# Optimization experiments

Hardware: AMD Instinct MI355X
Metric: run time of the kernel (lower is better)

The kernel has to match this reference:

```python
import jax, jax.numpy as jnp
import numpy as np

EMB, H, KV, HD = 2048, 32, 8, 64
G = H // KV  # group size = 4
SEQ, B = 2048, 1
EPS = 1e-6


def rms_norm(x, scale):
    # fp32 RMSNorm over last dim, no bias/centering
    v = jnp.mean(x.astype(jnp.float32) ** 2, axis=-1, keepdims=True)
    return (x * jax.lax.rsqrt(v + EPS) * scale).astype(x.dtype)


def apply_rope(x, cos, sin):
    # x: [b, h, s, d]; cos/sin: [s, d]
    d2 = x.shape[-1] // 2
    x1, x2 = x[..., :d2], x[..., d2:]
    rot = jnp.concatenate((-x2, x1), axis=-1)
    return (x * cos[None, None] + rot * sin[None, None]).astype(x.dtype)


def setup_inputs() -> dict:
    key = jax.random.key(0)
    ks = jax.random.split(key, 6)
    x = jax.random.normal(ks[0], (B, SEQ, EMB), jnp.float32)
    mask = jnp.triu(jnp.ones((SEQ, SEQ), jnp.bool_), k=1)  # causal: True = masked
    inv_freq = 1.0 / (10000.0 ** (np.arange(0, HD, 2, dtype=np.float32) / HD))
    t = np.arange(SEQ, dtype=np.float32)
    ang = np.outer(t, inv_freq)  # [seq, hd/2]
    ang = np.concatenate([ang, ang], axis=-1)  # [seq, hd]
    cos = jnp.asarray(np.cos(ang), jnp.float32)
    sin = jnp.asarray(np.sin(ang), jnp.float32)
    s = 0.02
    Wq = jax.random.normal(ks[1], (EMB, H * HD), jnp.float32) * s
    Wk = jax.random.normal(ks[2], (EMB, KV * HD), jnp.float32) * s
    Wv = jax.random.normal(ks[3], (EMB, KV * HD), jnp.float32) * s
    Wo = jax.random.normal(ks[4], (H * HD, EMB), jnp.float32) * s
    q_scale = jnp.ones((HD,), jnp.float32)
    k_scale = jnp.ones((HD,), jnp.float32)
    return {"x": x, "mask": mask, "cos": cos, "sin": sin, "Wq": Wq, "Wk": Wk,
            "Wv": Wv, "Wo": Wo, "q_scale": q_scale, "k_scale": k_scale}


def reference(x, mask, cos, sin, Wq, Wk, Wv, Wo, q_scale, k_scale):
    b, s, _ = x.shape
    q = (x @ Wq).reshape(b, s, H, HD).transpose(0, 2, 1, 3)     # [b,h,s,d]
    k = (x @ Wk).reshape(b, s, KV, HD).transpose(0, 2, 1, 3)    # [b,kv,s,d]
    v = (x @ Wv).reshape(b, s, KV, HD).transpose(0, 2, 1, 3)
    q = rms_norm(q, q_scale)
    k = rms_norm(k, k_scale)
    q = apply_rope(q, cos, sin)
    k = apply_rope(k, cos, sin)
    # grouped heads: h = kv*G + g (matches repeat_interleave along head dim)
    qg = q.reshape(b, KV, G, s, HD)
    scores = jnp.einsum('bkgqd,bkld->bkgql', qg, k) / jnp.sqrt(jnp.float32(HD))
    scores = jnp.where(mask[None, None, None], -jnp.inf, scores)
    w = jax.nn.softmax(scores.astype(jnp.float32), axis=-1).astype(q.dtype)
    ctx = jnp.einsum('bkgql,bkld->bkgqd', w, v)                 # [b,kv,g,s,d]
    ctx = ctx.reshape(b, H, s, HD).transpose(0, 2, 1, 3).reshape(b, s, H * HD)
    return ctx @ Wo
```

## Files before the change

### kernel.cpp

```cpp
#include <hip/hip_runtime.h>
#include <stdint.h>

#define EMB 2048
#define NH 32
#define NKV 8
#define HD 64
#define SEQ 2048
#define QKV_N 3072

using u16 = unsigned short;
typedef __attribute__((ext_vector_type(8))) short bf16x8;
typedef __attribute__((ext_vector_type(4))) float f32x4;
typedef __attribute__((ext_vector_type(4))) unsigned short u16x4;

__device__ inline u16 f2b(float f) {
  union { float f; unsigned u; } v; v.f = f;
  unsigned r = v.u + 0x7fffu + ((v.u >> 16) & 1u);
  return (u16)(r >> 16);
}

__device__ inline void gload16(const void* g, void* l) {
  __builtin_amdgcn_global_load_lds(
      (const __attribute__((address_space(1))) void*)g,
      (__attribute__((address_space(3))) void*)l, 16, 0, 0);
}

__global__ void cvt_x(const float* __restrict__ x, u16* __restrict__ xb) {
  int i = blockIdx.x * blockDim.x + threadIdx.x;
  float4 v = ((const float4*)x)[i];
  u16x4 o = { f2b(v.x), f2b(v.y), f2b(v.z), f2b(v.w) };
  ((u16x4*)xb)[i] = o;
}

__global__ void wtrans(const float* __restrict__ src, u16* __restrict__ dst, int R, int C) {
  __shared__ float t[64][65];
  int tx = threadIdx.x & 63, ty = threadIdx.x >> 6;
  int r0 = blockIdx.y * 64, c0 = blockIdx.x * 64;
#pragma unroll
  for (int i = 0; i < 16; ++i) {
    int r = ty * 16 + i;
    t[r][tx] = src[(size_t)(r0 + r) * C + c0 + tx];
  }
  __syncthreads();
#pragma unroll
  for (int i = 0; i < 16; ++i) {
    int r = ty * 16 + i;
    dst[(size_t)(c0 + r) * R + r0 + tx] = f2b(t[tx][r]);
  }
}

__global__ void wtrans_qkv(const float* __restrict__ Wq, const float* __restrict__ Wk,
                           const float* __restrict__ Wv, u16* __restrict__ dst) {
  __shared__ float t[64][65];
  int tx = threadIdx.x & 63, ty = threadIdx.x >> 6;
  int bx = blockIdx.x;
  int r0 = blockIdx.y * 64;
  const float* src; int C, c0;
  if (bx < 32)      { src = Wq; C = 2048; c0 = bx * 64; }
  else if (bx < 40) { src = Wk; C = 512;  c0 = (bx - 32) * 64; }
  else              { src = Wv; C = 512;  c0 = (bx - 40) * 64; }
#pragma unroll
  for (int i = 0; i < 16; ++i) {
    int r = ty * 16 + i;
    t[r][tx] = src[(size_t)(r0 + r) * C + c0 + tx];
  }
  __syncthreads();
  int drow = bx * 64;
#pragma unroll
  for (int i = 0; i < 16; ++i) {
    int r = ty * 16 + i;
    dst[(size_t)(drow + r) * 2048 + r0 + tx] = f2b(t[tx][r]);
  }
}

template<int OUT_MODE>
__global__ __launch_bounds__(256, 2)
void gemm_bt(const u16* __restrict__ A, const u16* __restrict__ BT,
             float* __restrict__ Cp, int M, int N, int K, int nwgy,
             const float* __restrict__ cosT, const float* __restrict__ sinT,
             const float* __restrict__ qsc, const float* __restrict__ ksc,
             u16* __restrict__ qb, u16* __restrict__ kb, u16* __restrict__ vT) {
  __shared__ u16 As[2][128 * 64];
  __shared__ u16 Bs[2][128 * 64];
  const int tid = threadIdx.x;
  const int w = tid >> 6, lane = tid & 63;
  const int lr = lane & 15, lg = lane >> 4;
  const int nwg = gridDim.x, cpx = nwg >> 3, pos = blockIdx.x;
  const int o = (pos & 7) * cpx + (pos >> 3);
  const int by = o % nwgy, bx = o / nwgy;
  const int m0 = by * 128, n0 = bx * 128;
  const int wm = (w >> 1) * 64, wn = (w & 1) * 64;
  f32x4 acc[4][4] = {};
  const int nk = K >> 6;

  auto STAGE = [&](int buf, int kt) {
    const int k0 = kt << 6;
    const int j = tid & 7;
#pragma unroll
    for (int i = 0; i < 4; ++i) {
      int r = i * 32 + (tid >> 3);
      int sc = (j ^ (r & 7)) * 8;
      gload16(&A[(size_t)(m0 + r) * K + k0 + sc], (char*)As[buf] + i * 4096 + w * 1024);
      gload16(&BT[(size_t)(n0 + r) * K + k0 + sc], (char*)Bs[buf] + i * 4096 + w * 1024);
    }
  };

  int cur = 0;
  STAGE(0, 0);
  asm volatile("s_waitcnt vmcnt(0)" ::: "memory");
  __syncthreads();
  for (int kt = 0; kt < nk; ++kt) {
    if (kt + 1 < nk) STAGE(cur ^ 1, kt + 1);
#pragma unroll
    for (int ks = 0; ks < 2; ++ks) {
      bf16x8 a[4], b[4];
#pragma unroll
      for (int i = 0; i < 4; ++i) {
        int row = wm + i * 16 + lr;
        a[i] = *(const bf16x8*)&As[cur][row * 64 + ((ks * 4 + lg) ^ (row & 7)) * 8];
      }
#pragma unroll
      for (int j = 0; j < 4; ++j) {
        int row = wn + j * 16 + lr;
        b[j] = *(const bf16x8*)&Bs[cur][row * 64 + ((ks * 4 + lg) ^ (row & 7)) * 8];
      }
#pragma unroll
      for (int i = 0; i < 4; ++i)
#pragma unroll
        for (int j = 0; j < 4; ++j)
          acc[i][j] = __builtin_amdgcn_mfma_f32_16x16x32_bf16(a[i], b[j], acc[i][j], 0, 0, 0);
    }
    asm volatile("s_waitcnt vmcnt(0)" ::: "memory");
    __syncthreads();
    cur ^= 1;
  }

  if (OUT_MODE == 0) {
#pragma unroll
    for (int i = 0; i < 4; ++i)
#pragma unroll
      for (int j = 0; j < 4; ++j)
#pragma unroll
        for (int r = 0; r < 4; ++r) {
          int row = m0 + wm + i * 16 + lg * 4 + r;
          int col = n0 + wn + j * 16 + lr;
          Cp[(size_t)row * N + col] = acc[i][j][r];
        }
  } else {
    const int hh = (n0 + wn) >> 6;
    if (hh < 40) {
      const float* scp = (hh < 32) ? qsc : ksc;
      u16* dst = (hh < 32) ? (qb + (size_t)hh * SEQ * HD)
                           : (kb + (size_t)(hh - 32) * SEQ * HD);
      const float qmul = (hh < 32) ? 0.125f : 1.0f;
#pragma unroll
      for (int i = 0; i < 4; ++i)
#pragma unroll
        for (int r = 0; r < 4; ++r) {
          float ssq = 0.f;
#pragma unroll
          for (int j = 0; j < 4; ++j) ssq += acc[i][j][r] * acc[i][j][r];
          ssq += __shfl_xor(ssq, 1);
          ssq += __shfl_xor(ssq, 2);
          ssq += __shfl_xor(ssq, 4);
          ssq += __shfl_xor(ssq, 8);
          float rs = rsqrtf(ssq * (1.0f / 64.0f) + 1e-6f);
          int s = m0 + wm + i * 16 + lg * 4 + r;
          float xn[4];
#pragma unroll
          for (int j = 0; j < 4; ++j) xn[j] = acc[i][j][r] * rs * scp[j * 16 + lr];
#pragma unroll
          for (int j = 0; j < 2; ++j) {
            int d = j * 16 + lr;
            float o1 = (xn[j] * cosT[s * 64 + d] - xn[j + 2] * sinT[s * 64 + d]) * qmul;
            float o2 = (xn[j + 2] * cosT[s * 64 + 32 + d] + xn[j] * sinT[s * 64 + 32 + d]) * qmul;
            dst[(size_t)s * 64 + d] = f2b(o1);
            dst[(size_t)s * 64 + 32 + d] = f2b(o2);
          }
        }
    } else {
      const int kvh = hh - 40;
      const int sbase = m0 + wm + lg * 4;
#pragma unroll
      for (int i = 0; i < 4; ++i)
#pragma unroll
        for (int j = 0; j < 4; ++j) {
          int d = j * 16 + lr;
          u16x4 pk = { f2b(acc[i][j][0]), f2b(acc[i][j][1]),
                       f2b(acc[i][j][2]), f2b(acc[i][j][3]) };
          *(u16x4*)&vT[((size_t)kvh * HD + d) * SEQ + sbase + i * 16] = pk;
        }
    }
  }
}

template<bool MASKED>
__device__ __forceinline__ void attn_step(
    const u16* __restrict__ Ks, const u16* __restrict__ VTs, u16* __restrict__ Psw,
    bf16x8 q0, bf16x8 q1, f32x4* O, float* l_acc,
    int qbase, int kbase, int lr, int lg) {
  f32x4 sc[4];
#pragma unroll
  for (int kj = 0; kj < 4; ++kj) {
    int r2 = kj * 16 + lr, sw = r2 & 7;
    bf16x8 kf0 = *(const bf16x8*)&Ks[r2 * 64 + (lg ^ sw) * 8];
    bf16x8 kf1 = *(const bf16x8*)&Ks[r2 * 64 + ((4 + lg) ^ sw) * 8];
    f32x4 z = {};
    z = __builtin_amdgcn_mfma_f32_16x16x32_bf16(q0, kf0, z, 0, 0, 0);
    z = __builtin_amdgcn_mfma_f32_16x16x32_bf16(q1, kf1, z, 0, 0, 0);
    sc[kj] = z;
  }
#pragma unroll
  for (int kj = 0; kj < 4; ++kj)
#pragma unroll
    for (int r = 0; r < 4; ++r) {
      float p;
      if (MASKED) {
        int qg = qbase + lg * 4 + r;
        int kg = kbase + kj * 16 + lr;
        p = (kg > qg) ? 0.0f : __expf(sc[kj][r] - 8.0f);
      } else {
        p = __expf(sc[kj][r] - 8.0f);
      }
      l_acc[r] += p;
      int row = lg * 4 + r, col = kj * 16 + lr;
      int sj = (col >> 3) ^ (row & 7);
      Psw[row * 64 + sj * 8 + (col & 7)] = f2b(p);
    }
#pragma unroll
  for (int ks2 = 0; ks2 < 2; ++ks2) {
    bf16x8 pa = *(const bf16x8*)&Psw[lr * 64 + ((ks2 * 4 + lg) ^ (lr & 7)) * 8];
#pragma unroll
    for (int n = 0; n < 4; ++n) {
      int r3 = n * 16 + lr, sw3 = r3 & 7;
      bf16x8 vb = *(const bf16x8*)&VTs[r3 * 64 + ((ks2 * 4 + lg) ^ sw3) * 8];
      O[n] = __builtin_amdgcn_mfma_f32_16x16x32_bf16(pa, vb, O[n], 0, 0, 0);
    }
  }
}

__global__ __launch_bounds__(256, 2)
void attn(const u16* __restrict__ qb, const u16* __restrict__ kb,
          const u16* __restrict__ vT, u16* __restrict__ ctx) {
  __shared__ u16 Ks[2][64 * 64];
  __shared__ u16 VTs[2][64 * 64];
  __shared__ u16 Ps[4][16 * 64];
  const int tid = threadIdx.x, w = tid >> 6, lane = tid & 63;
  const int lr = lane & 15, lg = lane >> 4;
  const int pos = blockIdx.x;
  const int o = (pos & 7) * 64 + (pos >> 3);
  const int h = o >> 4, p = o & 15;
  const int kvh = h >> 2;
  const int qtA = p, qtB = 31 - p;
  const int qbaseA = qtA * 64 + w * 16, qbaseB = qtB * 64 + w * 16;
  u16* Psw = &Ps[w][0];

  bf16x8 qA0 = *(const bf16x8*)&qb[((size_t)h * SEQ + qbaseA + lr) * HD + lg * 8];
  bf16x8 qA1 = *(const bf16x8*)&qb[((size_t)h * SEQ + qbaseA + lr) * HD + 32 + lg * 8];
  bf16x8 qB0 = *(const bf16x8*)&qb[((size_t)h * SEQ + qbaseB + lr) * HD + lg * 8];
  bf16x8 qB1 = *(const bf16x8*)&qb[((size_t)h * SEQ + qbaseB + lr) * HD + 32 + lg * 8];

  f32x4 OA[4] = {}, OB[4] = {};
  float lA[4] = {0.f, 0.f, 0.f, 0.f}, lB[4] = {0.f, 0.f, 0.f, 0.f};

  auto STAGE = [&](int buf, int kt) {
    const int kbase = kt * 64;
#pragma unroll
    for (int i = 0; i < 2; ++i) {
      int c = i * 256 + tid;
      int r = c >> 3, j = c & 7, sj = j ^ (r & 7);
      gload16(&kb[((size_t)kvh * SEQ + kbase + r) * HD + sj * 8],
              (char*)Ks[buf] + i * 4096 + w * 1024);
      gload16(&vT[((size_t)kvh * HD + r) * SEQ + kbase + sj * 8],
              (char*)VTs[buf] + i * 4096 + w * 1024);
    }
  };

  int cur = 0;
  STAGE(0, 0);
  asm volatile("s_waitcnt vmcnt(0)" ::: "memory");
  __syncthreads();
  for (int kt = 0; kt <= qtB; ++kt) {
    if (kt < qtB) STAGE(cur ^ 1, kt + 1);
    const int kbase = kt * 64;
    if (kt <= qtA) {
      if (kt == qtA)
        attn_step<true >(Ks[cur], VTs[cur], Psw, qA0, qA1, OA, lA, qbaseA, kbase, lr, lg);
      else
        attn_step<false>(Ks[cur], VTs[cur], Psw, qA0, qA1, OA, lA, qbaseA, kbase, lr, lg);
    }
    if (kt == qtB)
      attn_step<true >(Ks[cur], VTs[cur], Psw, qB0, qB1, OB, lB, qbaseB, kbase, lr, lg);
    else
      attn_step<false>(Ks[cur], VTs[cur], Psw, qB0, qB1, OB, lB, qbaseB, kbase, lr, lg);
    asm volatile("s_waitcnt vmcnt(0)" ::: "memory");
    __syncthreads();
    cur ^= 1;
  }

#pragma unroll
  for (int r = 0; r < 4; ++r) {
#pragma unroll
    for (int off = 1; off < 16; off <<= 1) {
      lA[r] += __shfl_xor(lA[r], off);
      lB[r] += __shfl_xor(lB[r], off);
    }
  }
#pragma unroll
  for (int n = 0; n < 4; ++n)
#pragma unroll
    for (int r = 0; r < 4; ++r) {
      int sA = qbaseA + lg * 4 + r;
      ctx[(size_t)sA * 2048 + h * 64 + n * 16 + lr] = f2b(OA[n][r] / lA[r]);
      int sB = qbaseB + lg * 4 + r;
      ctx[(size_t)sB * 2048 + h * 64 + n * 16 + lr] = f2b(OB[n][r] / lB[r]);
    }
}

extern "C" void kernel_launch(void* const* d_in, const int* in_sizes, int n_in,
                              void* d_out, int out_size, void* d_ws, size_t ws_size,
                              hipStream_t stream) {
  const float* x    = (const float*)d_in[0];
  const float* cosT = (const float*)d_in[2];
  const float* sinT = (const float*)d_in[3];
  const float* Wq   = (const float*)d_in[4];
  const float* Wk   = (const float*)d_in[5];
  const float* Wv   = (const float*)d_in[6];
  const float* Wo   = (const float*)d_in[7];
  const float* qsc  = (const float*)d_in[8];
  const float* ksc  = (const float*)d_in[9];
  float* out = (float*)d_out;

  char* wsp = (char*)d_ws;
  u16*   xb    = (u16*)(wsp);
  u16*   WqkvT = (u16*)(wsp + ((size_t)8  << 20));
  u16*   WoT   = (u16*)(wsp + ((size_t)20 << 20));
  u16*   qbuf  = (u16*)(wsp + ((size_t)28 << 20));
  u16*   kbuf  = (u16*)(wsp + ((size_t)36 << 20));
  u16*   vTbuf = (u16*)(wsp + ((size_t)38 << 20));
  u16*   ctxb  = (u16*)(wsp + ((size_t)40 << 20));

  cvt_x<<<4096, 256, 0, stream>>>(x, xb);
  wtrans_qkv<<<dim3(48, 32), 256, 0, stream>>>(Wq, Wk, Wv, WqkvT);
  wtrans<<<dim3(32, 32), 256, 0, stream>>>(Wo, WoT, 2048, 2048);

  gemm_bt<2><<<384, 256, 0, stream>>>(xb, WqkvT, nullptr, 2048, 3072, 2048, 16,
                                      cosT, sinT, qsc, ksc, qbuf, kbuf, vTbuf);
  attn<<<512, 256, 0, stream>>>(qbuf, kbuf, vTbuf, ctxb);
  gemm_bt<0><<<256, 256, 0, stream>>>((const u16*)ctxb, WoT, out, 2048, 2048, 2048, 16,
                                      nullptr, nullptr, nullptr, nullptr,
                                      nullptr, nullptr, nullptr);
}
```

Before: 139.4 us.

## Deepen attention K/V prefetch to 4 buffers and share K/V fragments across tiles

The attention loop now uses four LDS buffers for K and V with a prefetch distance of two tiles, waiting on partial vmcnt instead of draining all loads each iteration. The two query tiles (A and B) are processed in one fused step, so each K/V fragment is read from LDS once and feeds both sets of MFMAs. Softmax switches to exp2 with log2(e) folded into the Q scaling, and the P conversion to bf16 uses a cheaper rounding. The goal is less load-latency stall and fewer LDS reads. The cost is more LDS per block (80KB), which may limit occupancy, and slightly different rounding of P.

```diff
diff --git a/kernel.cpp b/kernel.cpp
--- a/kernel.cpp
+++ b/kernel.cpp
@@ -13,10 +13,17 @@
 typedef __attribute__((ext_vector_type(4))) float f32x4;
 typedef __attribute__((ext_vector_type(4))) unsigned short u16x4;
 
+#define MFMA16(a, b, c) __builtin_amdgcn_mfma_f32_16x16x32_bf16(a, b, c, 0, 0, 0)
+#define EXP2_C8 11.5415603f
+
 __device__ inline u16 f2b(float f) {
   union { float f; unsigned u; } v; v.f = f;
   unsigned r = v.u + 0x7fffu + ((v.u >> 16) & 1u);
   return (u16)(r >> 16);
+}
+__device__ inline u16 f2b_fast(float f) {
+  union { float f; unsigned u; } v; v.f = f;
+  return (u16)((v.u + 0x8000u) >> 16);
 }
 
 __device__ inline void gload16(const void* g, void* l) {
@@ -128,7 +135,7 @@
       for (int i = 0; i < 4; ++i)
 #pragma unroll
         for (int j = 0; j < 4; ++j)
-          acc[i][j] = __builtin_amdgcn_mfma_f32_16x16x32_bf16(a[i], b[j], acc[i][j], 0, 0, 0);
+          acc[i][j] = MFMA16(a[i], b[j], acc[i][j]);
     }
     asm volatile("s_waitcnt vmcnt(0)" ::: "memory");
     __syncthreads();
@@ -152,7 +159,7 @@
       const float* scp = (hh < 32) ? qsc : ksc;
       u16* dst = (hh < 32) ? (qb + (size_t)hh * SEQ * HD)
                            : (kb + (size_t)(hh - 32) * SEQ * HD);
-      const float qmul = (hh < 32) ? 0.125f : 1.0f;
+      const float qmul = (hh < 32) ? 0.18033688f : 1.0f;
 #pragma unroll
       for (int i = 0; i < 4; ++i)
 #pragma unroll
@@ -194,47 +201,70 @@
   }
 }
 
-template<bool MASKED>
-__device__ __forceinline__ void attn_step(
-    const u16* __restrict__ Ks, const u16* __restrict__ VTs, u16* __restrict__ Psw,
-    bf16x8 q0, bf16x8 q1, f32x4* O, float* l_acc,
-    int qbase, int kbase, int lr, int lg) {
-  f32x4 sc[4];
+template<int DOA, int MA, int MB>
+__device__ __forceinline__ void attn_step2(
+    const u16* __restrict__ Kc, const u16* __restrict__ Vc,
+    u16* __restrict__ PsA, u16* __restrict__ PsB,
+    const bf16x8& qA0, const bf16x8& qA1, const bf16x8& qB0, const bf16x8& qB1,
+    f32x4* OA, f32x4* OB, float* lA, float* lB,
+    int qbaseA, int qbaseB, int kbase, int lr, int lg) {
+  f32x4 scA[4], scB[4];
 #pragma unroll
   for (int kj = 0; kj < 4; ++kj) {
     int r2 = kj * 16 + lr, sw = r2 & 7;
-    bf16x8 kf0 = *(const bf16x8*)&Ks[r2 * 64 + (lg ^ sw) * 8];
-    bf16x8 kf1 = *(const bf16x8*)&Ks[r2 * 64 + ((4 + lg) ^ sw) * 8];
+    bf16x8 kf0 = *(const bf16x8*)&Kc[r2 * 64 + (lg ^ sw) * 8];
+    bf16x8 kf1 = *(const bf16x8*)&Kc[r2 * 64 + ((4 + lg) ^ sw) * 8];
     f32x4 z = {};
-    z = __builtin_amdgcn_mfma_f32_16x16x32_bf16(q0, kf0, z, 0, 0, 0);
-    z = __builtin_amdgcn_mfma_f32_16x16x32_bf16(q1, kf1, z, 0, 0, 0);
-    sc[kj] = z;
+    z = MFMA16(qB0, kf0, z);
+    z = MFMA16(qB1, kf1, z);
+    scB[kj] = z;
+    if (DOA) {
+      f32x4 y = {};
+      y = MFMA16(qA0, kf0, y);
+      y = MFMA16(qA1, kf1, y);
+      scA[kj] = y;
+    }
   }
 #pragma unroll
   for (int kj = 0; kj < 4; ++kj)
 #pragma unroll
     for (int r = 0; r < 4; ++r) {
-      float p;
-      if (MASKED) {
-        int qg = qbase + lg * 4 + r;
-        int kg = kbase + kj * 16 + lr;
-        p = (kg > qg) ? 0.0f : __expf(sc[kj][r] - 8.0f);
-      } else {
-        p = __expf(sc[kj][r] - 8.0f);
+      int row = lg * 4 + r, col = kj * 16 + lr;
+      int addr = row * 64 + (((col >> 3) ^ (row & 7)) * 8) + (col & 7);
+      {
+        float p;
+        if (MB) {
+          int kg = kbase + col, qg = qbaseB + row;
+          p = (kg > qg) ? 0.0f : exp2f(scB[kj][r] - EXP2_C8);
+        } else {
+          p = exp2f(scB[kj][r] - EXP2_C8);
+        }
+        lB[r] += p;
+        PsB[addr] = f2b_fast(p);
       }
-      l_acc[r] += p;
-      int row = lg * 4 + r, col = kj * 16 + lr;
-      int sj = (col >> 3) ^ (row & 7);
-      Psw[row * 64 + sj * 8 + (col & 7)] = f2b(p);
+      if (DOA) {
+        float p;
+        if (MA) {
+          int kg = kbase + col, qg = qbaseA + row;
+          p = (kg > qg) ? 0.0f : exp2f(scA[kj][r] - EXP2_C8);
+        } else {
+          p = exp2f(scA[kj][r] - EXP2_C8);
+        }
+        lA[r] += p;
+        PsA[addr] = f2b_fast(p);
+      }
     }
 #pragma unroll
   for (int ks2 = 0; ks2 < 2; ++ks2) {
-    bf16x8 pa = *(const bf16x8*)&Psw[lr * 64 + ((ks2 * 4 + lg) ^ (lr & 7)) * 8];
+    bf16x8 paB = *(const bf16x8*)&PsB[lr * 64 + ((ks2 * 4 + lg) ^ (lr & 7)) * 8];
+    bf16x8 paA;
+    if (DOA) paA = *(const bf16x8*)&PsA[lr * 64 + ((ks2 * 4 + lg) ^ (lr & 7)) * 8];
 #pragma unroll
     for (int n = 0; n < 4; ++n) {
       int r3 = n * 16 + lr, sw3 = r3 & 7;
-      bf16x8 vb = *(const bf16x8*)&VTs[r3 * 64 + ((ks2 * 4 + lg) ^ sw3) * 8];
-      O[n] = __builtin_amdgcn_mfma_f32_16x16x32_bf16(pa, vb, O[n], 0, 0, 0);
+      bf16x8 vb = *(const bf16x8*)&Vc[r3 * 64 + ((ks2 * 4 + lg) ^ sw3) * 8];
+      OB[n] = MFMA16(paB, vb, OB[n]);
+      if (DOA) OA[n] = MFMA16(paA, vb, OA[n]);
     }
   }
 }
@@ -242,9 +272,9 @@
 __global__ __launch_bounds__(256, 2)
 void attn(const u16* __restrict__ qb, const u16* __restrict__ kb,
           const u16* __restrict__ vT, u16* __restrict__ ctx) {
-  __shared__ u16 Ks[2][64 * 64];
-  __shared__ u16 VTs[2][64 * 64];
-  __shared__ u16 Ps[4][16 * 64];
+  __shared__ u16 Ks[4][64 * 64];
+  __shared__ u16 VTs[4][64 * 64];
+  __shared__ u16 Ps[4][2][16 * 64];
   const int tid = threadIdx.x, w = tid >> 6, lane = tid & 63;
   const int lr = lane & 15, lg = lane >> 4;
   const int pos = blockIdx.x;
@@ -253,7 +283,8 @@
   const int kvh = h >> 2;
   const int qtA = p, qtB = 31 - p;
   const int qbaseA = qtA * 64 + w * 16, qbaseB = qtB * 64 + w * 16;
-  u16* Psw = &Ps[w][0];
+  u16* PsA = &Ps[w][0][0];
+  u16* PsB = &Ps[w][1][0];
 
   bf16x8 qA0 = *(const bf16x8*)&qb[((size_t)h * SEQ + qbaseA + lr) * HD + lg * 8];
   bf16x8 qA1 = *(const bf16x8*)&qb[((size_t)h * SEQ + qbaseA + lr) * HD + 32 + lg * 8];
@@ -276,26 +307,30 @@
     }
   };
 
-  int cur = 0;
   STAGE(0, 0);
-  asm volatile("s_waitcnt vmcnt(0)" ::: "memory");
-  __syncthreads();
+  STAGE(1, 1);
   for (int kt = 0; kt <= qtB; ++kt) {
-    if (kt < qtB) STAGE(cur ^ 1, kt + 1);
+    const int rem = qtB - kt;
+    if (rem >= 2) STAGE((kt + 2) & 3, kt + 2);
+    if (rem >= 2)      asm volatile("s_waitcnt vmcnt(8)" ::: "memory");
+    else if (rem == 1) asm volatile("s_waitcnt vmcnt(4)" ::: "memory");
+    else               asm volatile("s_waitcnt vmcnt(0)" ::: "memory");
+    __syncthreads();
+    const u16* Kc = &Ks[kt & 3][0];
+    const u16* Vc = &VTs[kt & 3][0];
     const int kbase = kt * 64;
-    if (kt <= qtA) {
-      if (kt == qtA)
-        attn_step<true >(Ks[cur], VTs[cur], Psw, qA0, qA1, OA, lA, qbaseA, kbase, lr, lg);
-      else
-        attn_step<false>(Ks[cur], VTs[cur], Psw, qA0, qA1, OA, lA, qbaseA, kbase, lr, lg);
-    }
-    if (kt == qtB)
-      attn_step<true >(Ks[cur], VTs[cur], Psw, qB0, qB1, OB, lB, qbaseB, kbase, lr, lg);
+    if (kt < qtA)
+      attn_step2<1, 0, 0>(Kc, Vc, PsA, PsB, qA0, qA1, qB0, qB1, OA, OB, lA, lB,
+                          qbaseA, qbaseB, kbase, lr, lg);
+    else if (kt == qtA)
+      attn_step2<1, 1, 0>(Kc, Vc, PsA, PsB, qA0, qA1, qB0, qB1, OA, OB, lA, lB,
+                          qbaseA, qbaseB, kbase, lr, lg);
+    else if (kt < qtB)
+      attn_step2<0, 0, 0>(Kc, Vc, PsA, PsB, qA0, qA1, qB0, qB1, OA, OB, lA, lB,
+                          qbaseA, qbaseB, kbase, lr, lg);
     else
-      attn_step<false>(Ks[cur], VTs[cur], Psw, qB0, qB1, OB, lB, qbaseB, kbase, lr, lg);
-    asm volatile("s_waitcnt vmcnt(0)" ::: "memory");
-    __syncthreads();
-    cur ^= 1;
+      attn_step2<0, 0, 1>(Kc, Vc, PsA, PsB, qA0, qA1, qB0, qB1, OA, OB, lA, lB,
+                          qbaseA, qbaseB, kbase, lr, lg);
   }
 
 #pragma unroll
```

Result: slower. 147.7 us (+5.9%).
